# Kernel optimization log

Measured on AMD Instinct MI355X. Metric: run time of the kernel, lower is better.

## Reference

```python
import jax, jax.numpy as jnp
import numpy as np

B, S, H, L = 64, 512, 768, 9


def setup_inputs() -> dict:
    key = jax.random.key(0)
    ks = jax.random.split(key, 8)
    hidden = jax.random.normal(ks[0], (B, S, H), jnp.float32)
    lengths = jax.random.randint(ks[1], (B,), S // 2, S + 1)
    attention_mask = (jnp.arange(S)[None, :] < lengths[:, None]).astype(jnp.int32)
    labels = jax.random.randint(ks[2], (B, S), 0, L)
    # sprinkle some -100 ignore labels like HF datasets do
    ignore = jax.random.uniform(ks[3], (B, S)) < 0.05
    labels = jnp.where(ignore, -100, labels)
    W = jax.random.normal(ks[4], (H, L), jnp.float32) * 0.02
    b = jnp.zeros((L,), jnp.float32)
    start_transitions = jax.random.uniform(ks[5], (L,), jnp.float32, -0.1, 0.1)
    end_transitions = jax.random.uniform(ks[6], (L,), jnp.float32, -0.1, 0.1)
    transitions = jax.random.uniform(ks[7], (L, L), jnp.float32, -0.1, 0.1)
    return dict(hidden=hidden, attention_mask=attention_mask, labels=labels, W=W, b=b,
                start_transitions=start_transitions, end_transitions=end_transitions,
                transitions=transitions)


def _crf_numerator(emissions, tags, maskf, start_t, end_t, trans):
    # score of the gold tag sequence (torchcrf _compute_score)
    first = start_t[tags[:, 0]] + jnp.take_along_axis(emissions[:, 0], tags[:, 0:1], axis=1)[:, 0]
    em = jnp.take_along_axis(emissions, tags[..., None], axis=2)[..., 0]      # [B,S]
    tr = trans[tags[:, :-1], tags[:, 1:]]                                     # [B,S-1]
    score = first + jnp.sum((em[:, 1:] + tr) * maskf[:, 1:], axis=1)
    last_idx = (jnp.sum(maskf, axis=1).astype(jnp.int32) - 1)
    last_tags = jnp.take_along_axis(tags, last_idx[:, None], axis=1)[:, 0]
    return score + end_t[last_tags]


def _crf_lognorm(emissions, maskf, start_t, end_t, trans):
    # forward algorithm (torchcrf _compute_normalizer) as a lax.scan
    score0 = start_t[None, :] + emissions[:, 0]                               # [B,L]
    em_seq = jnp.transpose(emissions[:, 1:], (1, 0, 2))                       # [S-1,B,L]
    m_seq = maskf[:, 1:].T                                                    # [S-1,B]

    def step(score, xs):
        em_t, m_t = xs
        nxt = jax.nn.logsumexp(score[:, :, None] + trans[None] + em_t[:, None, :], axis=1)
        return jnp.where(m_t[:, None] > 0, nxt, score), None

    score, _ = jax.lax.scan(step, score0, (em_seq, m_seq))
    return jax.nn.logsumexp(score + end_t[None, :], axis=1)


def _viterbi(emissions, maskf, start_t, end_t, trans):
    score0 = start_t[None, :] + emissions[:, 0]                               # [B,L]
    em_seq = jnp.transpose(emissions[:, 1:], (1, 0, 2))
    m_seq = maskf[:, 1:].T

    def step(score, xs):
        em_t, m_t = xs
        cand = score[:, :, None] + trans[None]                                # [B,L,L]
        bp = jnp.argmax(cand, axis=1)                                         # [B,L]
        nxt = jnp.max(cand, axis=1) + em_t
        return jnp.where(m_t[:, None] > 0, nxt, score), bp

    score, history = jax.lax.scan(step, score0, (em_seq, m_seq))              # history [S-1,B,L]
    best_last = jnp.argmax(score + end_t[None, :], axis=1)                    # [B]

    def back(cur, xs):
        bp_t, m_t = xs
        prev = jnp.where(m_t > 0, jnp.take_along_axis(bp_t, cur[:, None], axis=1)[:, 0], cur)
        return prev, prev

    _, tags_rev = jax.lax.scan(back, best_last, (history[::-1], m_seq[::-1]))
    tags = jnp.concatenate([tags_rev[::-1].T, best_last[:, None]], axis=1)    # [B,S]
    return tags


def reference(hidden, attention_mask, labels, W, b, start_transitions, end_transitions, transitions):
    maskf = attention_mask.astype(hidden.dtype)                               # [B,S]
    logits = jnp.einsum('bsh,hl->bsl', hidden, W) + b                         # [B,S,L]
    safe_labels = jnp.where(labels == -100, 0, labels)
    num = _crf_numerator(logits, safe_labels, maskf, start_transitions, end_transitions, transitions)
    den = _crf_lognorm(logits, maskf, start_transitions, end_transitions, transitions)
    loss = -jnp.mean(num - den)                                               # -crf(..., reduction='mean')
    tags = _viterbi(logits, maskf, start_transitions, end_transitions, transitions)
    fake_logits = jax.nn.one_hot(tags, L, dtype=logits.dtype) * maskf[..., None]
    return loss, fake_logits
```

## Files before the change

kernel.cpp:

```cpp
#include <hip/hip_runtime.h>
#include <hip/hip_bf16.h>
#include <stdint.h>

constexpr int BB  = 64;
constexpr int SS  = 512;
constexpr int HH  = 768;
constexpr int NL  = 9;
constexpr int NROWS = BB * SS;
constexpr int EMN   = SS * NL;
constexpr int NSEG  = 8;
constexpr float NEG  = -1e30f;

__device__ __forceinline__ float readlane_f(float v, int lane) {
  union { float f; int i; } u;
  u.f = v;
  u.i = __builtin_amdgcn_readlane(u.i, lane);
  return u.f;
}

__global__ __launch_bounds__(256, 2) void logits_kernel(
    const float* __restrict__ hidden, const float* __restrict__ W,
    const float* __restrict__ bias, const int* __restrict__ mask,
    float* __restrict__ logits, int* __restrict__ lens) {
  const int lane = threadIdx.x & 63;
  const int wid  = blockIdx.x * 4 + (threadIdx.x >> 6);

  if (blockIdx.x < 64 && threadIdx.x < 64) {
    const int4* mp = (const int4*)(mask + blockIdx.x * SS);
    const int4 a = mp[threadIdx.x];
    const int4 c = mp[threadIdx.x + 64];
    int lsum = a.x + a.y + a.z + a.w + c.x + c.y + c.z + c.w;
#pragma unroll
    for (int off = 32; off >= 1; off >>= 1) lsum += __shfl_xor(lsum, off, 64);
    if (threadIdx.x == 0) lens[blockIdx.x] = lsum;
  }

  float w[3][4][NL];
#pragma unroll
  for (int j = 0; j < 3; ++j)
#pragma unroll
    for (int k = 0; k < 4; ++k) {
      const int r = lane * 4 + j * 256 + k;
#pragma unroll
      for (int l = 0; l < NL; ++l) w[j][k][l] = W[r * NL + l];
    }
  const float my_bias = (lane < NL) ? bias[lane] : 0.0f;

  float4 h[4][3];
#pragma unroll
  for (int r = 0; r < 4; ++r) {
    const float4* hp = (const float4*)(hidden + (size_t)(wid + r * 8192) * HH);
#pragma unroll
    for (int j = 0; j < 3; ++j) h[r][j] = hp[lane + j * 64];
  }
  float acc[4][NL];
#pragma unroll
  for (int r = 0; r < 4; ++r)
#pragma unroll
    for (int l = 0; l < NL; ++l) acc[r][l] = 0.0f;
#pragma unroll
  for (int r = 0; r < 4; ++r)
#pragma unroll
    for (int j = 0; j < 3; ++j)
#pragma unroll
      for (int l = 0; l < NL; ++l)
        acc[r][l] += h[r][j].x * w[j][0][l] + h[r][j].y * w[j][1][l] +
                     h[r][j].z * w[j][2][l] + h[r][j].w * w[j][3][l];
#pragma unroll
  for (int off = 32; off >= 1; off >>= 1)
#pragma unroll
    for (int r = 0; r < 4; ++r)
#pragma unroll
      for (int l = 0; l < NL; ++l)
        acc[r][l] += __shfl_xor(acc[r][l], off, 64);
  if (lane < NL) {
#pragma unroll
    for (int r = 0; r < 4; ++r) {
      float v = acc[r][0];
#pragma unroll
      for (int l = 1; l < NL; ++l) if (lane == l) v = acc[r][l];
      logits[(size_t)(wid + r * 8192) * NL + lane] = v + my_bias;
    }
  }
}

__global__ __launch_bounds__(64) void scan_kernel(
    const float* __restrict__ logits, const int* __restrict__ labels,
    const float* __restrict__ start_t, const float* __restrict__ end_t,
    const float* __restrict__ trans, float* __restrict__ out,
    float* __restrict__ num_den, const int* __restrict__ lens,
    float* __restrict__ segmat) {
  __shared__ unsigned char bp_s[EMN + 80];
  __shared__ unsigned char tags_s[SS];
  __shared__ int lab[SS];

  const int blk = blockIdx.x;
  const int tid = threadIdx.x;
  const int j   = (tid < NL) ? tid : NL - 1;

  if (blk < 64) {
    const int b   = blk;
    const int len = lens[b];
    const float* emb = logits + (size_t)b * EMN;
    float tc[NL];
#pragma unroll
    for (int i = 0; i < NL; ++i) tc[i] = trans[i * NL + j];
    float s[NL];
#pragma unroll
    for (int i = 0; i < NL; ++i) s[i] = start_t[i] + emb[i];
    float eA = emb[1 * NL + j], eB = emb[2 * NL + j];
    float eC = emb[3 * NL + j], eD = emb[4 * NL + j];
    for (int t = 1; t < len; ++t) {
      float c[NL];
#pragma unroll
      for (int i = 0; i < NL; ++i) c[i] = s[i] + tc[i];
      const float x01 = fmaxf(c[0], c[1]), x23 = fmaxf(c[2], c[3]);
      const float x45 = fmaxf(c[4], c[5]), x67 = fmaxf(c[6], c[7]);
      const float best = fmaxf(fmaxf(fmaxf(x01, x23), fmaxf(x45, x67)), c[8]);
      const float nxt = best + eA;
      {
        const bool b01 = c[0] >= c[1], b23 = c[2] >= c[3];
        const bool b45 = c[4] >= c[5], b67 = c[6] >= c[7];
        const float v01 = b01 ? c[0] : c[1]; const int i01 = b01 ? 0 : 1;
        const float v23 = b23 ? c[2] : c[3]; const int i23 = b23 ? 2 : 3;
        const float v45 = b45 ? c[4] : c[5]; const int i45 = b45 ? 4 : 5;
        const float v67 = b67 ? c[6] : c[7]; const int i67 = b67 ? 6 : 7;
        const bool bA = v01 >= v23, bB = v45 >= v67;
        const float vA = bA ? v01 : v23; const int iA = bA ? i01 : i23;
        const float vB = bB ? v45 : v67; const int iB = bB ? i45 : i67;
        const bool bC = vA >= vB;
        const float vC = bC ? vA : vB; const int iC = bC ? iA : iB;
        const bool bD = vC >= c[8];
        const int arg = bD ? iC : 8;
        bp_s[t * NL + tid] = (unsigned char)arg;
      }
#pragma unroll
      for (int i = 0; i < NL; ++i) s[i] = readlane_f(nxt, i);
      eA = eB; eB = eC; eC = eD;
      eD = emb[(t + 4) * NL + j];
    }
    float bv = s[0] + end_t[0];
    int   bl = 0;
#pragma unroll
    for (int i = 1; i < NL; ++i) {
      const float cc = s[i] + end_t[i];
      if (cc > bv) { bv = cc; bl = i; }
    }
    __syncthreads();

    uint64_t C = 0x876543210ULL;
#pragma unroll
    for (int k = 1; k <= 8; ++k) {
      const int t = 8 * tid + k;
      uint64_t nc = 0;
#pragma unroll
      for (int x = 0; x < 9; ++x) {
        const int g = bp_s[t * NL + x] & 15;
        nc |= ((C >> (4 * g)) & 15ULL) << (4 * x);
      }
      C = (t < len) ? nc : C;
    }
    const uint32_t Clo = (uint32_t)C, Chi = (uint32_t)(C >> 32);
    uint32_t cur = (uint32_t)bl;
    int bnd = 0;
#pragma unroll
    for (int c = 63; c >= 0; --c) {
      bnd = (tid == c) ? (int)cur : bnd;
      const uint32_t lo = (uint32_t)__builtin_amdgcn_readlane((int)Clo, c);
      const uint32_t hi = (uint32_t)__builtin_amdgcn_readlane((int)Chi, c);
      const uint64_t cc = ((uint64_t)hi << 32) | lo;
      cur = (uint32_t)((cc >> (4 * cur)) & 15u);
    }
    int tag = bnd;
#pragma unroll
    for (int k = 8; k >= 1; --k) {
      const int t = 8 * tid + k;
      const int tt = (t < 512) ? t : 511;
      const int nt = bp_s[tt * NL + tag];
      tag = (t < len) ? nt : tag;
      tags_s[t - 1] = (unsigned char)tag;
    }
    __syncthreads();
    for (int i = tid; i < EMN; i += 64) {
      const int t = i / NL;
      const int l = i - t * NL;
      out[1 + (size_t)b * EMN + i] =
          (t < len && l == (int)tags_s[t]) ? 1.0f : 0.0f;
    }

  } else if (blk < 128) {
    const int b   = blk - 64;
    const int len = lens[b];
    const float* emb = logits + (size_t)b * EMN;
    for (int t = tid; t < SS; t += 64) {
      const int v = labels[b * SS + t];
      lab[t] = (v == -100) ? 0 : v;
    }
    __syncthreads();
    float contrib = 0.0f;
    for (int t = tid; t < SS; t += 64) {
      if (t >= 1 && t < len)
        contrib += emb[t * NL + lab[t]] + trans[lab[t - 1] * NL + lab[t]];
    }
#pragma unroll
    for (int off = 32; off >= 1; off >>= 1)
      contrib += __shfl_xor(contrib, off, 64);
    if (tid == 0) {
      const int l0 = lab[0];
      num_den[b] = start_t[l0] + emb[l0] + contrib + end_t[lab[len - 1]];
    }

  } else {
    const int id   = blk - 128;
    const int pair = id / 3;
    const int wv   = id - pair * 3;
    const int b    = pair >> 3;
    const int sg   = pair & 7;
    const int e0   = 3 * wv;
    const int len  = lens[b];
    const float* emb = logits + (size_t)b * EMN;
    float tc[NL];
#pragma unroll
    for (int i = 0; i < NL; ++i) tc[i] = trans[i * NL + j];
    float s0[NL], s1[NL], s2[NL];
#pragma unroll
    for (int i = 0; i < NL; ++i) {
      s0[i] = (i == e0)     ? 0.0f : NEG;
      s1[i] = (i == e0 + 1) ? 0.0f : NEG;
      s2[i] = (i == e0 + 2) ? 0.0f : NEG;
    }
    float my0 = (j == e0)     ? 0.0f : NEG;
    float my1 = (j == e0 + 1) ? 0.0f : NEG;
    float my2 = (j == e0 + 2) ? 0.0f : NEG;
    const int tbeg  = 64 * sg + 1;
    const int tlast = (64 * sg + 64 < 511) ? 64 * sg + 64 : 511;
    float eA = emb[tbeg * NL + j],       eB = emb[(tbeg + 1) * NL + j];
    float eC = emb[(tbeg + 2) * NL + j], eD = emb[(tbeg + 3) * NL + j];
    for (int t = tbeg; t <= tlast; ++t) {
      if (t >= len) break;
      float c0[NL], c1[NL], c2[NL];
#pragma unroll
      for (int i = 0; i < NL; ++i) {
        c0[i] = s0[i] + tc[i];
        c1[i] = s1[i] + tc[i];
        c2[i] = s2[i] + tc[i];
      }
      const float m0 = fmaxf(fmaxf(fmaxf(fmaxf(c0[0], c0[1]), fmaxf(c0[2], c0[3])),
                                   fmaxf(fmaxf(c0[4], c0[5]), fmaxf(c0[6], c0[7]))), c0[8]);
      const float m1 = fmaxf(fmaxf(fmaxf(fmaxf(c1[0], c1[1]), fmaxf(c1[2], c1[3])),
                                   fmaxf(fmaxf(c1[4], c1[5]), fmaxf(c1[6], c1[7]))), c1[8]);
      const float m2 = fmaxf(fmaxf(fmaxf(fmaxf(c2[0], c2[1]), fmaxf(c2[2], c2[3])),
                                   fmaxf(fmaxf(c2[4], c2[5]), fmaxf(c2[6], c2[7]))), c2[8]);
      float u0 = 0.0f, u1 = 0.0f, u2 = 0.0f;
#pragma unroll
      for (int i = 0; i < NL; ++i) {
        u0 += __expf(c0[i] - m0);
        u1 += __expf(c1[i] - m1);
        u2 += __expf(c2[i] - m2);
      }
      my0 = m0 + __logf(u0) + eA;
      my1 = m1 + __logf(u1) + eA;
      my2 = m2 + __logf(u2) + eA;
#pragma unroll
      for (int i = 0; i < NL; ++i) {
        s0[i] = readlane_f(my0, i);
        s1[i] = readlane_f(my1, i);
        s2[i] = readlane_f(my2, i);
      }
      eA = eB; eB = eC; eC = eD;
      eD = emb[(t + 4) * NL + j];
    }
    if (tid < NL) {
      float* M = segmat + (size_t)(b * NSEG + sg) * 81;
      M[(e0    ) * NL + tid] = my0;
      M[(e0 + 1) * NL + tid] = my1;
      M[(e0 + 2) * NL + tid] = my2;
    }
  }
}

__global__ __launch_bounds__(64) void combine_kernel(
    const float* __restrict__ logits, const float* __restrict__ segmat,
    const float* __restrict__ start_t, const float* __restrict__ end_t,
    const float* __restrict__ num_den, float* __restrict__ out) {
  const int b   = blockIdx.x;
  const int tid = threadIdx.x;
  const int j   = (tid < NL) ? tid : NL - 1;
  float s[NL];
#pragma unroll
  for (int i = 0; i < NL; ++i) s[i] = start_t[i] + logits[(size_t)b * EMN + i];
  float mcur[NL], mnxt[NL];
  {
    const float* M = segmat + (size_t)(b * NSEG) * 81;
#pragma unroll
    for (int i = 0; i < NL; ++i) mcur[i] = M[i * NL + j];
  }
  for (int sg = 0; sg < NSEG; ++sg) {
    if (sg + 1 < NSEG) {
      const float* M = segmat + (size_t)(b * NSEG + sg + 1) * 81;
#pragma unroll
      for (int i = 0; i < NL; ++i) mnxt[i] = M[i * NL + j];
    }
    float c[NL];
#pragma unroll
    for (int i = 0; i < NL; ++i) c[i] = s[i] + mcur[i];
    const float x01 = fmaxf(c[0], c[1]), x23 = fmaxf(c[2], c[3]);
    const float x45 = fmaxf(c[4], c[5]), x67 = fmaxf(c[6], c[7]);
    const float m = fmaxf(fmaxf(fmaxf(x01, x23), fmaxf(x45, x67)), c[8]);
    float sum = 0.0f;
#pragma unroll
    for (int i = 0; i < NL; ++i) sum += __expf(c[i] - m);
    const float nxt = m + __logf(sum);
#pragma unroll
    for (int i = 0; i < NL; ++i) s[i] = readlane_f(nxt, i);
#pragma unroll
    for (int i = 0; i < NL; ++i) mcur[i] = mnxt[i];
  }
  float c[NL];
#pragma unroll
  for (int i = 0; i < NL; ++i) c[i] = s[i] + end_t[i];
  const float x01 = fmaxf(c[0], c[1]), x23 = fmaxf(c[2], c[3]);
  const float x45 = fmaxf(c[4], c[5]), x67 = fmaxf(c[6], c[7]);
  const float m = fmaxf(fmaxf(fmaxf(x01, x23), fmaxf(x45, x67)), c[8]);
  float sum = 0.0f;
#pragma unroll
  for (int i = 0; i < NL; ++i) sum += __expf(c[i] - m);
  if (tid == 0) {
    const float den = m + __logf(sum);
    atomicAdd(out, (den - num_den[b]) * (1.0f / 64.0f));
  }
}

extern "C" void kernel_launch(void* const* d_in, const int* in_sizes, int n_in,
                              void* d_out, int out_size, void* d_ws, size_t ws_size,
                              hipStream_t stream) {
  const float* hidden  = (const float*)d_in[0];
  const int*   mask    = (const int*)d_in[1];
  const int*   labels  = (const int*)d_in[2];
  const float* W       = (const float*)d_in[3];
  const float* bias    = (const float*)d_in[4];
  const float* start_t = (const float*)d_in[5];
  const float* end_t   = (const float*)d_in[6];
  const float* trans   = (const float*)d_in[7];
  float* out = (float*)d_out;

  float* logits  = (float*)d_ws;
  float* segmat  = logits + (size_t)NROWS * NL;
  float* num_den = segmat + (size_t)BB * NSEG * 81;
  int*   lens    = (int*)(num_den + 128);

  hipMemsetAsync(out, 0, sizeof(float), stream);
  logits_kernel<<<2048, 256, 0, stream>>>(hidden, W, bias, mask, logits, lens);
  scan_kernel<<<1664, 64, 0, stream>>>(logits, labels, start_t, end_t, trans,
                                       out, num_den, lens, segmat);
  combine_kernel<<<64, 64, 0, stream>>>(logits, segmat, start_t, end_t,
                                        num_den, out);
}
```

Before: 258.5 us.

## Stage weights and emissions in LDS and simplify Viterbi argmax

The logits kernel now copies W into shared memory in a per-lane layout and reads it back as float4 vectors, instead of having every thread load its own weight slice straight from global memory. The Viterbi scan stages each batch's emission row into LDS up front, so the serial loop no longer pays global-load latency on every step. The argmax tree is replaced by an equality bitmask followed by find-first-set. This adds LDS footprint and a block barrier, and the LDS use may cut occupancy in the logits kernel.

```diff
diff --git a/kernel.cpp b/kernel.cpp
--- a/kernel.cpp
+++ b/kernel.cpp
@@ -22,29 +22,29 @@
     const float* __restrict__ hidden, const float* __restrict__ W,
     const float* __restrict__ bias, const int* __restrict__ mask,
     float* __restrict__ logits, int* __restrict__ lens) {
-  const int lane = threadIdx.x & 63;
-  const int wid  = blockIdx.x * 4 + (threadIdx.x >> 6);
-
-  if (blockIdx.x < 64 && threadIdx.x < 64) {
+  __shared__ float wlds[64 * 144];
+  const int tid  = threadIdx.x;
+  const int lane = tid & 63;
+  const int wid  = blockIdx.x * 4 + (tid >> 6);
+
+  if (blockIdx.x < 64 && tid < 64) {
     const int4* mp = (const int4*)(mask + blockIdx.x * SS);
-    const int4 a = mp[threadIdx.x];
-    const int4 c = mp[threadIdx.x + 64];
+    const int4 a = mp[tid];
+    const int4 c = mp[tid + 64];
     int lsum = a.x + a.y + a.z + a.w + c.x + c.y + c.z + c.w;
 #pragma unroll
     for (int off = 32; off >= 1; off >>= 1) lsum += __shfl_xor(lsum, off, 64);
-    if (threadIdx.x == 0) lens[blockIdx.x] = lsum;
-  }
-
-  float w[3][4][NL];
-#pragma unroll
-  for (int j = 0; j < 3; ++j)
-#pragma unroll
-    for (int k = 0; k < 4; ++k) {
-      const int r = lane * 4 + j * 256 + k;
-#pragma unroll
-      for (int l = 0; l < NL; ++l) w[j][k][l] = W[r * NL + l];
-    }
+    if (tid == 0) lens[blockIdx.x] = lsum;
+  }
+
+  for (int it = tid; it < HH * NL; it += 256) {
+    const int e = it / NL, l = it - e * NL;
+    const int ln = (e & 255) >> 2, j = e >> 8, k = e & 3;
+    wlds[ln * 144 + j * 48 + k * 12 + l] = W[it];
+  }
+  __syncthreads();
   const float my_bias = (lane < NL) ? bias[lane] : 0.0f;
+  const float* wbase = wlds + lane * 144;
 
   float4 h[4][3];
 #pragma unroll
@@ -58,14 +58,34 @@
   for (int r = 0; r < 4; ++r)
 #pragma unroll
     for (int l = 0; l < NL; ++l) acc[r][l] = 0.0f;
-#pragma unroll
-  for (int r = 0; r < 4; ++r)
-#pragma unroll
-    for (int j = 0; j < 3; ++j)
-#pragma unroll
-      for (int l = 0; l < NL; ++l)
-        acc[r][l] += h[r][j].x * w[j][0][l] + h[r][j].y * w[j][1][l] +
-                     h[r][j].z * w[j][2][l] + h[r][j].w * w[j][3][l];
+
+#pragma unroll
+  for (int j = 0; j < 3; ++j) {
+#pragma unroll
+    for (int lq = 0; lq < 2; ++lq) {
+      const float4 w0 = *(const float4*)(wbase + j * 48 + 0 * 12 + lq * 4);
+      const float4 w1 = *(const float4*)(wbase + j * 48 + 1 * 12 + lq * 4);
+      const float4 w2 = *(const float4*)(wbase + j * 48 + 2 * 12 + lq * 4);
+      const float4 w3 = *(const float4*)(wbase + j * 48 + 3 * 12 + lq * 4);
+#pragma unroll
+      for (int r = 0; r < 4; ++r) {
+        const float4 hv = h[r][j];
+        acc[r][lq * 4 + 0] += hv.x * w0.x + hv.y * w1.x + hv.z * w2.x + hv.w * w3.x;
+        acc[r][lq * 4 + 1] += hv.x * w0.y + hv.y * w1.y + hv.z * w2.y + hv.w * w3.y;
+        acc[r][lq * 4 + 2] += hv.x * w0.z + hv.y * w1.z + hv.z * w2.z + hv.w * w3.z;
+        acc[r][lq * 4 + 3] += hv.x * w0.w + hv.y * w1.w + hv.z * w2.w + hv.w * w3.w;
+      }
+    }
+    const float w80 = wbase[j * 48 + 0 * 12 + 8];
+    const float w81 = wbase[j * 48 + 1 * 12 + 8];
+    const float w82 = wbase[j * 48 + 2 * 12 + 8];
+    const float w83 = wbase[j * 48 + 3 * 12 + 8];
+#pragma unroll
+    for (int r = 0; r < 4; ++r) {
+      const float4 hv = h[r][j];
+      acc[r][8] += hv.x * w80 + hv.y * w81 + hv.z * w82 + hv.w * w83;
+    }
+  }
 #pragma unroll
   for (int off = 32; off >= 1; off >>= 1)
 #pragma unroll
@@ -90,6 +110,7 @@
     const float* __restrict__ trans, float* __restrict__ out,
     float* __restrict__ num_den, const int* __restrict__ lens,
     float* __restrict__ segmat) {
+  __shared__ __align__(16) float em_s[EMN + 64];
   __shared__ unsigned char bp_s[EMN + 80];
   __shared__ unsigned char tags_s[SS];
   __shared__ int lab[SS];
@@ -101,15 +122,20 @@
   if (blk < 64) {
     const int b   = blk;
     const int len = lens[b];
-    const float* emb = logits + (size_t)b * EMN;
+    {
+      const float4* src = (const float4*)(logits + (size_t)b * EMN);
+      float4* dst = (float4*)em_s;
+      for (int i = tid; i < EMN / 4; i += 64) dst[i] = src[i];
+    }
     float tc[NL];
 #pragma unroll
     for (int i = 0; i < NL; ++i) tc[i] = trans[i * NL + j];
+    __syncthreads();
     float s[NL];
 #pragma unroll
-    for (int i = 0; i < NL; ++i) s[i] = start_t[i] + emb[i];
-    float eA = emb[1 * NL + j], eB = emb[2 * NL + j];
-    float eC = emb[3 * NL + j], eD = emb[4 * NL + j];
+    for (int i = 0; i < NL; ++i) s[i] = start_t[i] + em_s[i];
+    float eA = em_s[1 * NL + j], eB = em_s[2 * NL + j];
+    float eC = em_s[3 * NL + j], eD = em_s[4 * NL + j];
     for (int t = 1; t < len; ++t) {
       float c[NL];
 #pragma unroll
@@ -118,26 +144,14 @@
       const float x45 = fmaxf(c[4], c[5]), x67 = fmaxf(c[6], c[7]);
       const float best = fmaxf(fmaxf(fmaxf(x01, x23), fmaxf(x45, x67)), c[8]);
       const float nxt = best + eA;
-      {
-        const bool b01 = c[0] >= c[1], b23 = c[2] >= c[3];
-        const bool b45 = c[4] >= c[5], b67 = c[6] >= c[7];
-        const float v01 = b01 ? c[0] : c[1]; const int i01 = b01 ? 0 : 1;
-        const float v23 = b23 ? c[2] : c[3]; const int i23 = b23 ? 2 : 3;
-        const float v45 = b45 ? c[4] : c[5]; const int i45 = b45 ? 4 : 5;
-        const float v67 = b67 ? c[6] : c[7]; const int i67 = b67 ? 6 : 7;
-        const bool bA = v01 >= v23, bB = v45 >= v67;
-        const float vA = bA ? v01 : v23; const int iA = bA ? i01 : i23;
-        const float vB = bB ? v45 : v67; const int iB = bB ? i45 : i67;
-        const bool bC = vA >= vB;
-        const float vC = bC ? vA : vB; const int iC = bC ? iA : iB;
-        const bool bD = vC >= c[8];
-        const int arg = bD ? iC : 8;
-        bp_s[t * NL + tid] = (unsigned char)arg;
-      }
+      uint32_t eq = 0;
+#pragma unroll
+      for (int i = 0; i < NL; ++i) eq |= (c[i] == best) ? (1u << i) : 0u;
+      bp_s[t * NL + tid] = (unsigned char)(__ffs(eq) - 1);
 #pragma unroll
       for (int i = 0; i < NL; ++i) s[i] = readlane_f(nxt, i);
       eA = eB; eB = eC; eC = eD;
-      eD = emb[(t + 4) * NL + j];
+      eD = em_s[(t + 4) * NL + j];
     }
     float bv = s[0] + end_t[0];
     int   bl = 0;
```

After: 266.1 us. 2.9% more time.

## Rework logits GEMV via LDS tiles and defer Viterbi argmax to parallel phase

Applied to the files above, without the earlier changes.

The logits kernel now gives each thread one full row. A single-wave block stages 64x32 hidden tiles through LDS, with the next tile prefetched into registers, and W is read straight from global memory. This replaces the old wave-per-row layout that ended in a long shuffle reduction. The Viterbi scan now keeps only max scores on its serial critical path and stores the score vectors in LDS. Backpointer argmaxes are then recomputed in parallel across lanes and packed into nibble words, taking the compare/select chain off the sequential loop. The risks are that the logits kernel drops to 512 single-wave blocks, which may cut memory parallelism, and that backpointers computed after the scan must exactly match the original tie-breaking.

```diff
diff --git a/kernel.cpp b/kernel.cpp
--- a/kernel.cpp
+++ b/kernel.cpp
@@ -18,70 +18,60 @@
   return u.f;
 }
 
-__global__ __launch_bounds__(256, 2) void logits_kernel(
+__global__ __launch_bounds__(64) void logits_kernel(
     const float* __restrict__ hidden, const float* __restrict__ W,
     const float* __restrict__ bias, const int* __restrict__ mask,
     float* __restrict__ logits, int* __restrict__ lens) {
-  const int lane = threadIdx.x & 63;
-  const int wid  = blockIdx.x * 4 + (threadIdx.x >> 6);
-
-  if (blockIdx.x < 64 && threadIdx.x < 64) {
+  __shared__ float tile[64 * 33];
+  const int tid = threadIdx.x;
+
+  if (blockIdx.x < 64) {
     const int4* mp = (const int4*)(mask + blockIdx.x * SS);
-    const int4 a = mp[threadIdx.x];
-    const int4 c = mp[threadIdx.x + 64];
+    const int4 a = mp[tid];
+    const int4 c = mp[tid + 64];
     int lsum = a.x + a.y + a.z + a.w + c.x + c.y + c.z + c.w;
 #pragma unroll
     for (int off = 32; off >= 1; off >>= 1) lsum += __shfl_xor(lsum, off, 64);
-    if (threadIdx.x == 0) lens[blockIdx.x] = lsum;
-  }
-
-  float w[3][4][NL];
-#pragma unroll
-  for (int j = 0; j < 3; ++j)
-#pragma unroll
-    for (int k = 0; k < 4; ++k) {
-      const int r = lane * 4 + j * 256 + k;
-#pragma unroll
-      for (int l = 0; l < NL; ++l) w[j][k][l] = W[r * NL + l];
-    }
-  const float my_bias = (lane < NL) ? bias[lane] : 0.0f;
-
-  float4 h[4][3];
-#pragma unroll
-  for (int r = 0; r < 4; ++r) {
-    const float4* hp = (const float4*)(hidden + (size_t)(wid + r * 8192) * HH);
-#pragma unroll
-    for (int j = 0; j < 3; ++j) h[r][j] = hp[lane + j * 64];
-  }
-  float acc[4][NL];
-#pragma unroll
-  for (int r = 0; r < 4; ++r)
-#pragma unroll
-    for (int l = 0; l < NL; ++l) acc[r][l] = 0.0f;
-#pragma unroll
-  for (int r = 0; r < 4; ++r)
-#pragma unroll
-    for (int j = 0; j < 3; ++j)
-#pragma unroll
-      for (int l = 0; l < NL; ++l)
-        acc[r][l] += h[r][j].x * w[j][0][l] + h[r][j].y * w[j][1][l] +
-                     h[r][j].z * w[j][2][l] + h[r][j].w * w[j][3][l];
-#pragma unroll
-  for (int off = 32; off >= 1; off >>= 1)
-#pragma unroll
-    for (int r = 0; r < 4; ++r)
-#pragma unroll
-      for (int l = 0; l < NL; ++l)
-        acc[r][l] += __shfl_xor(acc[r][l], off, 64);
-  if (lane < NL) {
-#pragma unroll
-    for (int r = 0; r < 4; ++r) {
-      float v = acc[r][0];
-#pragma unroll
-      for (int l = 1; l < NL; ++l) if (lane == l) v = acc[r][l];
-      logits[(size_t)(wid + r * 8192) * NL + lane] = v + my_bias;
-    }
-  }
+    if (tid == 0) lens[blockIdx.x] = lsum;
+  }
+
+  const int rowbase = blockIdx.x * 64;
+  const float* hbase = hidden + (size_t)rowbase * HH;
+  float acc[NL];
+#pragma unroll
+  for (int l = 0; l < NL; ++l) acc[l] = 0.0f;
+
+  float r[32];
+#pragma unroll
+  for (int i = 0; i < 32; ++i) {
+    const int e = i * 64 + tid;
+    r[i] = hbase[(e >> 5) * HH + (e & 31)];
+  }
+  for (int c = 0; c < 24; ++c) {
+#pragma unroll
+    for (int i = 0; i < 32; ++i) {
+      const int e = i * 64 + tid;
+      tile[(e >> 5) * 33 + (e & 31)] = r[i];
+    }
+    if (c < 23) {
+      const float* hb = hbase + (c + 1) * 32;
+#pragma unroll
+      for (int i = 0; i < 32; ++i) {
+        const int e = i * 64 + tid;
+        r[i] = hb[(e >> 5) * HH + (e & 31)];
+      }
+    }
+    const float* wrow = W + c * 32 * NL;
+#pragma unroll
+    for (int k = 0; k < 32; ++k) {
+      const float h = tile[tid * 33 + k];
+#pragma unroll
+      for (int l = 0; l < NL; ++l) acc[l] += h * wrow[k * NL + l];
+    }
+  }
+  float* orow = logits + (size_t)(rowbase + tid) * NL;
+#pragma unroll
+  for (int l = 0; l < NL; ++l) orow[l] = acc[l] + bias[l];
 }
 
 __global__ __launch_bounds__(64) void scan_kernel(
@@ -90,64 +80,86 @@
     const float* __restrict__ trans, float* __restrict__ out,
     float* __restrict__ num_den, const int* __restrict__ lens,
     float* __restrict__ segmat) {
-  __shared__ unsigned char bp_s[EMN + 80];
-  __shared__ unsigned char tags_s[SS];
-  __shared__ int lab[SS];
+  __shared__ __align__(16) unsigned char smem[19280];
 
   const int blk = blockIdx.x;
   const int tid = threadIdx.x;
   const int j   = (tid < NL) ? tid : NL - 1;
 
   if (blk < 64) {
+    float* svec = (float*)smem;
+    unsigned char* tags_s = smem + 18432;
+    float* tr_s = (float*)(smem + 18960);
     const int b   = blk;
     const int len = lens[b];
     const float* emb = logits + (size_t)b * EMN;
+    for (int i = tid; i < NL * NL; i += 64) tr_s[i] = trans[i];
     float tc[NL];
 #pragma unroll
     for (int i = 0; i < NL; ++i) tc[i] = trans[i * NL + j];
     float s[NL];
 #pragma unroll
     for (int i = 0; i < NL; ++i) s[i] = start_t[i] + emb[i];
+    {
+      const float myv = start_t[j] + emb[j];
+      if (tid < NL) svec[tid] = myv;
+    }
     float eA = emb[1 * NL + j], eB = emb[2 * NL + j];
     float eC = emb[3 * NL + j], eD = emb[4 * NL + j];
     for (int t = 1; t < len; ++t) {
       float c[NL];
 #pragma unroll
       for (int i = 0; i < NL; ++i) c[i] = s[i] + tc[i];
-      const float x01 = fmaxf(c[0], c[1]), x23 = fmaxf(c[2], c[3]);
-      const float x45 = fmaxf(c[4], c[5]), x67 = fmaxf(c[6], c[7]);
-      const float best = fmaxf(fmaxf(fmaxf(x01, x23), fmaxf(x45, x67)), c[8]);
+      const float m012 = fmaxf(fmaxf(c[0], c[1]), c[2]);
+      const float m345 = fmaxf(fmaxf(c[3], c[4]), c[5]);
+      const float m678 = fmaxf(fmaxf(c[6], c[7]), c[8]);
+      const float best = fmaxf(fmaxf(m012, m345), m678);
       const float nxt = best + eA;
-      {
-        const bool b01 = c[0] >= c[1], b23 = c[2] >= c[3];
-        const bool b45 = c[4] >= c[5], b67 = c[6] >= c[7];
-        const float v01 = b01 ? c[0] : c[1]; const int i01 = b01 ? 0 : 1;
-        const float v23 = b23 ? c[2] : c[3]; const int i23 = b23 ? 2 : 3;
-        const float v45 = b45 ? c[4] : c[5]; const int i45 = b45 ? 4 : 5;
-        const float v67 = b67 ? c[6] : c[7]; const int i67 = b67 ? 6 : 7;
+      if (tid < NL) svec[t * NL + tid] = nxt;
+#pragma unroll
+      for (int i = 0; i < NL; ++i) s[i] = readlane_f(nxt, i);
+      eA = eB; eB = eC; eC = eD;
+      eD = emb[(t + 4) * NL + j];
+    }
+    float bv = s[0] + end_t[0];
+    int   bl = 0;
+#pragma unroll
+    for (int i = 1; i < NL; ++i) {
+      const float cc = s[i] + end_t[i];
+      if (cc > bv) { bv = cc; bl = i; }
+    }
+    __syncthreads();
+
+    uint64_t bpt[9];
+#pragma unroll
+    for (int k = 1; k <= 8; ++k) {
+      const int t = 8 * tid + k;
+      float sp[NL];
+#pragma unroll
+      for (int i = 0; i < NL; ++i) sp[i] = svec[(t - 1) * NL + i];
+      uint64_t nib = 0;
+#pragma unroll
+      for (int jj = 0; jj < NL; ++jj) {
+        float cc[NL];
+#pragma unroll
+        for (int i = 0; i < NL; ++i) cc[i] = sp[i] + tr_s[i * NL + jj];
+        const bool b01 = cc[0] >= cc[1], b23 = cc[2] >= cc[3];
+        const bool b45 = cc[4] >= cc[5], b67 = cc[6] >= cc[7];
+        const float v01 = b01 ? cc[0] : cc[1]; const int i01 = b01 ? 0 : 1;
+        const float v23 = b23 ? cc[2] : cc[3]; const int i23 = b23 ? 2 : 3;
+        const float v45 = b45 ? cc[4] : cc[5]; const int i45 = b45 ? 4 : 5;
+        const float v67 = b67 ? cc[6] : cc[7]; const int i67 = b67 ? 6 : 7;
         const bool bA = v01 >= v23, bB = v45 >= v67;
         const float vA = bA ? v01 : v23; const int iA = bA ? i01 : i23;
         const float vB = bB ? v45 : v67; const int iB = bB ? i45 : i67;
         const bool bC = vA >= vB;
         const float vC = bC ? vA : vB; const int iC = bC ? iA : iB;
-        const bool bD = vC >= c[8];
+        const bool bD = vC >= cc[8];
         const int arg = bD ? iC : 8;
-        bp_s[t * NL + tid] = (unsigned char)arg;
-      }
-#pragma unroll
-      for (int i = 0; i < NL; ++i) s[i] = readlane_f(nxt, i);
-      eA = eB; eB = eC; eC = eD;
-      eD = emb[(t + 4) * NL + j];
-    }
-    float bv = s[0] + end_t[0];
-    int   bl = 0;
-#pragma unroll
-    for (int i = 1; i < NL; ++i) {
-      const float cc = s[i] + end_t[i];
-      if (cc > bv) { bv = cc; bl = i; }
-    }
-    __syncthreads();
-
+        nib |= (uint64_t)arg << (4 * jj);
+      }
+      bpt[k] = nib;
+    }
     uint64_t C = 0x876543210ULL;
 #pragma unroll
     for (int k = 1; k <= 8; ++k) {
@@ -155,7 +167,7 @@
       uint64_t nc = 0;
 #pragma unroll
       for (int x = 0; x < 9; ++x) {
-        const int g = bp_s[t * NL + x] & 15;
+        const int g = (int)((bpt[k] >> (4 * x)) & 15);
         nc |= ((C >> (4 * g)) & 15ULL) << (4 * x);
       }
       C = (t < len) ? nc : C;
@@ -175,8 +187,7 @@
 #pragma unroll
     for (int k = 8; k >= 1; --k) {
       const int t = 8 * tid + k;
-      const int tt = (t < 512) ? t : 511;
-      const int nt = bp_s[tt * NL + tag];
+      const int nt = (int)((bpt[k] >> (4 * tag)) & 15);
       tag = (t < len) ? nt : tag;
       tags_s[t - 1] = (unsigned char)tag;
     }
@@ -189,6 +200,7 @@
     }
 
   } else if (blk < 128) {
+    int* lab = (int*)smem;
     const int b   = blk - 64;
     const int len = lens[b];
     const float* emb = logits + (size_t)b * EMN;
@@ -350,7 +362,7 @@
   int*   lens    = (int*)(num_den + 128);
 
   hipMemsetAsync(out, 0, sizeof(float), stream);
-  logits_kernel<<<2048, 256, 0, stream>>>(hidden, W, bias, mask, logits, lens);
+  logits_kernel<<<512, 64, 0, stream>>>(hidden, W, bias, mask, logits, lens);
   scan_kernel<<<1664, 64, 0, stream>>>(logits, labels, start_t, end_t, trans,
                                        out, num_den, lens, segmat);
   combine_kernel<<<64, 64, 0, stream>>>(logits, segmat, start_t, end_t,
```

Result: slower. 331.5 us (+28.2%).

## Restructure logits GEMV: row-per-thread with transposed W in LDS

Applied to the files above, without the earlier changes.

Rewrites the logits kernel so each thread computes one row over a quarter of the hidden dimension, reading W from a transposed shared-memory copy and combining partial sums through LDS instead of wave shuffles. The aim is to remove the heavy cross-lane shuffle reduction and per-thread W register loading. In exchange, hidden reads become strided per lane (each lane walks its own row), which may reduce coalescing, and the grid shrinks to 512 blocks with larger LDS use.

```diff
diff --git a/kernel.cpp b/kernel.cpp
--- a/kernel.cpp
+++ b/kernel.cpp
@@ -18,69 +18,57 @@
   return u.f;
 }
 
-__global__ __launch_bounds__(256, 2) void logits_kernel(
+__global__ __launch_bounds__(256) void logits_kernel(
     const float* __restrict__ hidden, const float* __restrict__ W,
     const float* __restrict__ bias, const int* __restrict__ mask,
     float* __restrict__ logits, int* __restrict__ lens) {
-  const int lane = threadIdx.x & 63;
-  const int wid  = blockIdx.x * 4 + (threadIdx.x >> 6);
-
-  if (blockIdx.x < 64 && threadIdx.x < 64) {
+  __shared__ float wt[NL * HH];
+  __shared__ float part[4][64][10];
+  const int tid  = threadIdx.x;
+  const int lane = tid & 63;
+  const int seg  = tid >> 6;
+
+  if (blockIdx.x < 64 && tid < 64) {
     const int4* mp = (const int4*)(mask + blockIdx.x * SS);
-    const int4 a = mp[threadIdx.x];
-    const int4 c = mp[threadIdx.x + 64];
+    const int4 a = mp[tid];
+    const int4 c = mp[tid + 64];
     int lsum = a.x + a.y + a.z + a.w + c.x + c.y + c.z + c.w;
 #pragma unroll
     for (int off = 32; off >= 1; off >>= 1) lsum += __shfl_xor(lsum, off, 64);
-    if (threadIdx.x == 0) lens[blockIdx.x] = lsum;
-  }
-
-  float w[3][4][NL];
-#pragma unroll
-  for (int j = 0; j < 3; ++j)
-#pragma unroll
-    for (int k = 0; k < 4; ++k) {
-      const int r = lane * 4 + j * 256 + k;
-#pragma unroll
-      for (int l = 0; l < NL; ++l) w[j][k][l] = W[r * NL + l];
-    }
-  const float my_bias = (lane < NL) ? bias[lane] : 0.0f;
-
-  float4 h[4][3];
-#pragma unroll
-  for (int r = 0; r < 4; ++r) {
-    const float4* hp = (const float4*)(hidden + (size_t)(wid + r * 8192) * HH);
-#pragma unroll
-    for (int j = 0; j < 3; ++j) h[r][j] = hp[lane + j * 64];
-  }
-  float acc[4][NL];
-#pragma unroll
-  for (int r = 0; r < 4; ++r)
-#pragma unroll
-    for (int l = 0; l < NL; ++l) acc[r][l] = 0.0f;
-#pragma unroll
-  for (int r = 0; r < 4; ++r)
-#pragma unroll
-    for (int j = 0; j < 3; ++j)
-#pragma unroll
-      for (int l = 0; l < NL; ++l)
-        acc[r][l] += h[r][j].x * w[j][0][l] + h[r][j].y * w[j][1][l] +
-                     h[r][j].z * w[j][2][l] + h[r][j].w * w[j][3][l];
-#pragma unroll
-  for (int off = 32; off >= 1; off >>= 1)
-#pragma unroll
-    for (int r = 0; r < 4; ++r)
-#pragma unroll
-      for (int l = 0; l < NL; ++l)
-        acc[r][l] += __shfl_xor(acc[r][l], off, 64);
-  if (lane < NL) {
-#pragma unroll
-    for (int r = 0; r < 4; ++r) {
-      float v = acc[r][0];
-#pragma unroll
-      for (int l = 1; l < NL; ++l) if (lane == l) v = acc[r][l];
-      logits[(size_t)(wid + r * 8192) * NL + lane] = v + my_bias;
-    }
+    if (tid == 0) lens[blockIdx.x] = lsum;
+  }
+
+  for (int idx = tid; idx < HH * NL; idx += 256) {
+    const int k = idx / NL, l = idx - k * NL;
+    wt[l * HH + k] = W[idx];
+  }
+  __syncthreads();
+
+  const int row = blockIdx.x * 64 + lane;
+  const float4* hp = (const float4*)(hidden + (size_t)row * HH + seg * 192);
+  const float* wsegbase = wt + seg * 192;
+  float acc[NL];
+#pragma unroll
+  for (int l = 0; l < NL; ++l) acc[l] = 0.0f;
+
+#pragma unroll 4
+  for (int kb = 0; kb < 48; ++kb) {
+    const float4 h4 = hp[kb];
+#pragma unroll
+    for (int l = 0; l < NL; ++l) {
+      const float4 w4 = *(const float4*)(wsegbase + l * HH + kb * 4);
+      acc[l] += h4.x * w4.x + h4.y * w4.y + h4.z * w4.z + h4.w * w4.w;
+    }
+  }
+#pragma unroll
+  for (int l = 0; l < NL; ++l) part[seg][lane][l] = acc[l];
+  __syncthreads();
+
+  for (int idx = tid; idx < 64 * NL; idx += 256) {
+    const int r = idx / NL, l = idx - r * NL;
+    logits[(size_t)(blockIdx.x * 64 + r) * NL + l] =
+        ((part[0][r][l] + part[1][r][l]) + (part[2][r][l] + part[3][r][l])) +
+        bias[l];
   }
 }
 
@@ -350,7 +338,7 @@
   int*   lens    = (int*)(num_den + 128);
 
   hipMemsetAsync(out, 0, sizeof(float), stream);
-  logits_kernel<<<2048, 256, 0, stream>>>(hidden, W, bias, mask, logits, lens);
+  logits_kernel<<<512, 256, 0, stream>>>(hidden, W, bias, mask, logits, lens);
   scan_kernel<<<1664, 64, 0, stream>>>(logits, labels, start_t, end_t, trans,
                                        out, num_den, lens, segmat);
   combine_kernel<<<64, 64, 0, stream>>>(logits, segmat, start_t, end_t,
```

New measurement: 264.1 us. +2.1%, slower.
